# Kernel optimization log

Hardware: AMD Instinct MI355X
Metric: run time of the kernel (lower is better)

Reference implementation:

```python
import jax, jax.numpy as jnp
import numpy as np

EPS = 0.25  # diffusion-map epsilon

def setup_inputs() -> dict:
    key = jax.random.key(0)
    ks = jax.random.split(key, 6)
    B, N, F, L = 8, 2048, 256, 16
    s = lambda fan_in: 1.0 / np.sqrt(fan_in)
    return {
        "x":      jax.random.normal(ks[0], (B, N, F), dtype=jnp.float32),
        "proj_w": jax.random.normal(ks[1], (L, F), dtype=jnp.float32) * s(F),
        "proj_b": jnp.zeros((L,), dtype=jnp.float32),
        "pi_w1":  jax.random.normal(ks[2], (F, L), dtype=jnp.float32) * s(L),
        "pi_b1":  jnp.zeros((F,), dtype=jnp.float32),
        "pi_w2":  jax.random.normal(ks[3], (1, F), dtype=jnp.float32) * s(F),
        "pi_b2":  jnp.zeros((1,), dtype=jnp.float32),
        "dt":     jnp.array([0.1], dtype=jnp.float32),
    }

def reference(x, proj_w, proj_b, pi_w1, pi_b1, pi_w2, pi_b2, dt):
    # z = proj(x): [B, N, L]
    z = jnp.einsum("bnf,lf->bnl", x, proj_w) + proj_b
    # pairwise squared distances via expansion (avoids [B,N,N,L] intermediate)
    sq = jnp.sum(z * z, axis=-1)                              # [B, N]
    gram = jnp.einsum("bnl,bml->bnm", z, z)                   # [B, N, N]
    d2 = jnp.maximum(sq[:, :, None] + sq[:, None, :] - 2.0 * gram, 0.0)
    K = jnp.exp(-d2 / (4.0 * EPS))                            # K_epsilon [B,N,N]
    q = jnp.sum(K, axis=2)                                    # q_epsilon_tilde [B,N]
    # pi(z): MLP 16 -> 256 -> 1 with ReLU then Sigmoid
    h = jax.nn.relu(jnp.einsum("bnl,fl->bnf", z, pi_w1) + pi_b1)
    pi_v = jax.nn.sigmoid(jnp.einsum("bnf,of->bno", h, pi_w2) + pi_b2)[..., 0]  # [B,N]
    # K_tilde = K @ diag(pi/q): scale columns
    Kt = K * (pi_v / q)[:, None, :]                            # [B,N,N]
    row = jnp.sum(Kt, axis=2) + 1e-5                           # diag of D_tilde
    # L = (1/eps) * D_tilde^{-1} K_tilde - I ; inverse of diagonal = reciprocal
    # L @ x computed without materializing identity:
    Lx = (1.0 / EPS) * jnp.einsum("bnm,bmf->bnf", Kt / row[:, :, None], x) - x
    return x + dt[0] * Lx
```

## Files before the change

### kernel.cpp

```cpp
#include <hip/hip_runtime.h>
#include <hip/hip_bf16.h>

#define BATCH 8
#define NN    2048
#define FF    256
#define LL    16

typedef float f32x4 __attribute__((ext_vector_type(4)));
typedef short s16x8 __attribute__((ext_vector_type(8)));

static __device__ __forceinline__ unsigned short f2bf(float f) {
    return __builtin_bit_cast(unsigned short, __float2bfloat16(f));
}
static __device__ __forceinline__ float bf2f(unsigned short u) {
    unsigned int x = ((unsigned int)u) << 16;
    return __builtin_bit_cast(float, x);
}

typedef const __attribute__((address_space(1))) unsigned int glb_uint;
typedef __attribute__((address_space(3))) unsigned int lds_uint;
static __device__ __forceinline__ void gload_lds16(const void* g, void* l) {
    __builtin_amdgcn_global_load_lds((glb_uint*)g, (lds_uint*)l, 16, 0, 0);
}

__global__ __launch_bounds__(256) void fused_a_kernel(
    const float* __restrict__ x,
    const float* __restrict__ proj_w, const float* __restrict__ proj_b,
    const float* __restrict__ pi_w1,  const float* __restrict__ pi_b1,
    const float* __restrict__ pi_w2,  const float* __restrict__ pi_b2,
    unsigned short* __restrict__ xT,
    unsigned short* __restrict__ zbG,
    float* __restrict__ sqbuf,
    float* __restrict__ pibuf)
{
    const int bid = blockIdx.x;
    const int b = bid & 7, nt = bid >> 3;
    const int n0 = nt * 64;
    const int t = threadIdx.x;
    const int wv = t >> 6, ln = t & 63;

    const float* xb = x + (size_t)b * NN * FF;
    unsigned short* xTb = xT + (size_t)b * FF * NN;

    __shared__ unsigned short xbsh[64 * 264];
    __shared__ unsigned short Wbsh[16 * 264];
    __shared__ unsigned short W1bsh[256 * 24];
    __shared__ unsigned short zbsh[64 * 24];
    __shared__ float b1sh[256], w2sh[256], pbsh[16];

#pragma unroll
    for (int i = 0; i < 16; ++i) {
        const int idx = i * 256 + t;
        const int r = idx >> 6, cq = idx & 63;
        const float4 v = *(const float4*)(xb + (size_t)(n0 + r) * FF + cq * 4);
        ushort4 o; o.x = f2bf(v.x); o.y = f2bf(v.y); o.z = f2bf(v.z); o.w = f2bf(v.w);
        *(ushort4*)&xbsh[r * 264 + cq * 4] = o;
    }
    {
        const int l = t >> 4, fq = t & 15;
#pragma unroll
        for (int k2 = 0; k2 < 4; ++k2) {
            const float4 v = *(const float4*)(proj_w + l * FF + fq * 16 + k2 * 4);
            ushort4 o; o.x = f2bf(v.x); o.y = f2bf(v.y); o.z = f2bf(v.z); o.w = f2bf(v.w);
            *(ushort4*)&Wbsh[l * 264 + fq * 16 + k2 * 4] = o;
        }
    }
    {
#pragma unroll
        for (int k2 = 0; k2 < 4; ++k2) {
            const float4 v = *(const float4*)(pi_w1 + t * LL + k2 * 4);
            ushort4 o; o.x = f2bf(v.x); o.y = f2bf(v.y); o.z = f2bf(v.z); o.w = f2bf(v.w);
            *(ushort4*)&W1bsh[t * 24 + k2 * 4] = o;
        }
        b1sh[t] = pi_b1[t];
        w2sh[t] = pi_w2[t];
        if (t < 16) pbsh[t] = proj_b[t];
    }
    __syncthreads();

    f32x4 zacc = {0.f, 0.f, 0.f, 0.f};
#pragma unroll
    for (int g = 0; g < 8; ++g) {
        const s16x8 af = *(const s16x8*)&xbsh[(wv * 16 + (ln & 15)) * 264 + g * 32 + (ln >> 4) * 8];
        const s16x8 bf = *(const s16x8*)&Wbsh[(ln & 15) * 264 + g * 32 + (ln >> 4) * 8];
        zacc = __builtin_amdgcn_mfma_f32_16x16x32_bf16(af, bf, zacc, 0, 0, 0);
    }
    {
        const float pb = pbsh[ln & 15];
#pragma unroll
        for (int r = 0; r < 4; ++r) {
            const float zv = zacc[r] + pb;
            zbsh[(wv * 16 + (ln >> 4) * 4 + r) * 24 + (ln & 15)] = f2bf(zv);
        }
    }
    __syncthreads();

    if (t < 64) {
        unsigned short zr[16];
        float sq = 0.f;
#pragma unroll
        for (int l = 0; l < 16; ++l) {
            zr[l] = zbsh[t * 24 + l];
            const float zf = bf2f(zr[l]);
            sq = fmaf(zf, zf, sq);
        }
        const size_t gz = ((size_t)b * NN + n0 + t) * 16;
#pragma unroll
        for (int q4 = 0; q4 < 4; ++q4)
            *(ushort4*)(zbG + gz + q4 * 4) = *(ushort4*)&zr[q4 * 4];
        sqbuf[(size_t)b * NN + n0 + t] = sq;
    }

    {
        s16x8 bz = {0, 0, 0, 0, 0, 0, 0, 0};
        if ((ln >> 4) < 2)
            bz = *(const s16x8*)&zbsh[(wv * 16 + (ln & 15)) * 24 + (ln >> 4) * 8];
        float pisum = 0.f;
        const f32x4 zf4 = {0.f, 0.f, 0.f, 0.f};
#pragma unroll
        for (int ft = 0; ft < 16; ++ft) {
            s16x8 aw = {0, 0, 0, 0, 0, 0, 0, 0};
            if ((ln >> 4) < 2)
                aw = *(const s16x8*)&W1bsh[(ft * 16 + (ln & 15)) * 24 + (ln >> 4) * 8];
            const f32x4 h4 = __builtin_amdgcn_mfma_f32_16x16x32_bf16(aw, bz, zf4, 0, 0, 0);
#pragma unroll
            for (int r = 0; r < 4; ++r) {
                const int f = ft * 16 + (ln >> 4) * 4 + r;
                float h = h4[r] + b1sh[f];
                h = fmaxf(h, 0.f);
                pisum = fmaf(h, w2sh[f], pisum);
            }
        }
        pisum += __shfl_xor(pisum, 16, 64);
        pisum += __shfl_xor(pisum, 32, 64);
        if (ln < 16) {
            const float tp = pisum + pi_b2[0];
            pibuf[(size_t)b * NN + n0 + wv * 16 + ln] = 1.f / (1.f + __expf(-tp));
        }
    }

    {
        const int foff = wv * 64;
#pragma unroll
        for (int ff = 0; ff < 64; ++ff) {
            const unsigned short v = xbsh[ln * 264 + foff + ff];
            xTb[(size_t)(foff + ff) * NN + n0 + ln] = v;
        }
    }
}

__global__ __launch_bounds__(256) void qc_kernel(
    const unsigned short* __restrict__ zbG,
    const float* __restrict__ sqbuf,
    const float* __restrict__ pibuf,
    float* __restrict__ cbuf)
{
    const int bid = blockIdx.x;
    const int b = bid & 7, nt = bid >> 3;
    const int n0 = nt * 64;
    const int t = threadIdx.x;
    const int wv = t >> 6, ln = t & 63;

    const unsigned short* zb = zbG + (size_t)b * NN * LL;
    const float* sqb = sqbuf + (size_t)b * NN;

    __shared__ unsigned short zq[2][256 * 24];
    __shared__ float sqq[2][256];

    s16x8 af = {0, 0, 0, 0, 0, 0, 0, 0};
    if ((ln >> 4) < 2)
        af = *(const s16x8*)(zb + (size_t)(n0 + wv * 16 + (ln & 15)) * 16 + (ln >> 4) * 8);
    float sqn[4];
#pragma unroll
    for (int r = 0; r < 4; ++r) sqn[r] = sqb[n0 + wv * 16 + (ln >> 4) * 4 + r];

    float S[4] = {0.f, 0.f, 0.f, 0.f};
    const f32x4 zf4 = {0.f, 0.f, 0.f, 0.f};

    uint4 za, zc; float sv;
    za = *(const uint4*)(zb + (size_t)t * 16);
    zc = *(const uint4*)(zb + (size_t)t * 16 + 8);
    sv = sqb[t];
    *(uint4*)&zq[0][t * 24] = za;
    *(uint4*)&zq[0][t * 24 + 8] = zc;
    sqq[0][t] = sv;
    __syncthreads();

    for (int ch = 0; ch < 8; ++ch) {
        const int cur = ch & 1;
        if (ch < 7) {
            const int m = (ch + 1) * 256 + t;
            za = *(const uint4*)(zb + (size_t)m * 16);
            zc = *(const uint4*)(zb + (size_t)m * 16 + 8);
            sv = sqb[m];
        }
#pragma unroll
        for (int mt = 0; mt < 16; ++mt) {
            const int mloc = mt * 16 + (ln & 15);
            s16x8 bf = {0, 0, 0, 0, 0, 0, 0, 0};
            if ((ln >> 4) < 2)
                bf = *(const s16x8*)&zq[cur][mloc * 24 + (ln >> 4) * 8];
            const f32x4 g = __builtin_amdgcn_mfma_f32_16x16x32_bf16(af, bf, zf4, 0, 0, 0);
            const float sqm = sqq[cur][mloc];
#pragma unroll
            for (int r = 0; r < 4; ++r)
                S[r] += __expf(2.f * g[r] - sqn[r] - sqm);
        }
        if (ch < 7) {
            *(uint4*)&zq[cur ^ 1][t * 24] = za;
            *(uint4*)&zq[cur ^ 1][t * 24 + 8] = zc;
            sqq[cur ^ 1][t] = sv;
        }
        __syncthreads();
    }
#pragma unroll
    for (int r = 0; r < 4; ++r) {
        S[r] += __shfl_xor(S[r], 1, 64);
        S[r] += __shfl_xor(S[r], 2, 64);
        S[r] += __shfl_xor(S[r], 4, 64);
        S[r] += __shfl_xor(S[r], 8, 64);
    }
    if ((ln & 15) == 0) {
#pragma unroll
        for (int r = 0; r < 4; ++r) {
            const int n = n0 + wv * 16 + (ln >> 4) * 4 + r;
            const size_t gi = (size_t)b * NN + n;
            cbuf[gi] = pibuf[gi] / S[r];
        }
    }
}

__global__ __launch_bounds__(512) void main_kernel(
    const float* __restrict__ x,
    const unsigned short* __restrict__ xT,
    const unsigned short* __restrict__ zbG,
    const float* __restrict__ sqbuf,
    const float* __restrict__ cbuf,
    const float* __restrict__ dtp,
    float* __restrict__ out)
{
    const int bid = blockIdx.x;
    const int b = bid & 7, nt = bid >> 3;
    const int n0 = nt * 64;
    const int t = threadIdx.x;
    const int wv = t >> 6, ln = t & 63;

    const float*          xb  = x   + (size_t)b * NN * FF;
    const unsigned short* xTb = xT  + (size_t)b * FF * NN;
    const unsigned short* zb  = zbG + (size_t)b * NN * LL;
    const float*          sqB = sqbuf + (size_t)b * NN;
    const float*          cB  = cbuf  + (size_t)b * NN;
    float*                ob  = out + (size_t)b * NN * FF;

    __shared__ unsigned short xsh[2 * 16384];
    __shared__ unsigned short wsh[2 * 4096];
    __shared__ unsigned short zsh[2 * 64 * 24];
    __shared__ float csh[2][64], sqh[2][64];
    __shared__ float rsp[2][64];

    const float dtv = dtp[0];
    const int ntile = wv >> 1;

    s16x8 af = {0, 0, 0, 0, 0, 0, 0, 0};
    if ((ln >> 4) < 2)
        af = *(const s16x8*)(zb + (size_t)(n0 + ntile * 16 + (ln & 15)) * 16 + (ln >> 4) * 8);
    float sqn[4];
#pragma unroll
    for (int r = 0; r < 4; ++r) sqn[r] = sqB[n0 + ntile * 16 + (ln >> 4) * 4 + r];

    f32x4 acc[2][4];
#pragma unroll
    for (int fi = 0; fi < 2; ++fi)
#pragma unroll
        for (int ni = 0; ni < 4; ++ni) acc[fi][ni] = (f32x4){0.f, 0.f, 0.f, 0.f};
    float rloc[4] = {0.f, 0.f, 0.f, 0.f};
    const f32x4 zf4 = {0.f, 0.f, 0.f, 0.f};

    uint4 zreg; float creg = 0.f, sreg = 0.f;

    if (t < 128) {
        const int m = t >> 1, half = t & 1;
        zreg = *(const uint4*)(zb + (size_t)m * 16 + half * 8);
        *(uint4*)&zsh[m * 24 + half * 8] = zreg;
    } else if (t < 192) {
        csh[0][t - 128] = cB[t - 128];
    } else if (t < 256) {
        sqh[0][t - 192] = sqB[t - 192];
    }
#pragma unroll
    for (int i = 0; i < 4; ++i) {
        const int floc = i * 8 + (ln >> 3);
        const int cp = ln & 7;
        const int cl = cp ^ (floc & 7);
        const unsigned short* src = xTb + (size_t)(wv * 32 + floc) * NN + cl * 8;
        gload_lds16(src, (char*)xsh + wv * 4096 + i * 1024);
    }
    __syncthreads();

    for (int kt = 0; kt < 32; ++kt) {
        const int cur = kt & 1;
        unsigned short* zc = zsh + cur * (64 * 24);
        unsigned short* wc = wsh + cur * 4096;
        const unsigned short* xc = xsh + cur * 16384;

        if (kt < 31) {
            const int m1 = (kt + 1) * 64;
            if (t < 128) {
                const int m = t >> 1, half = t & 1;
                zreg = *(const uint4*)(zb + (size_t)(m1 + m) * 16 + half * 8);
            } else if (t < 192) creg = cB[m1 + t - 128];
            else if (t < 256)   sreg = sqB[m1 + t - 192];
        }

#pragma unroll
        for (int mi = 0; mi < 2; ++mi) {
            const int mt = (wv & 1) * 2 + mi;
            const int mloc = mt * 16 + (ln & 15);
            s16x8 bf = {0, 0, 0, 0, 0, 0, 0, 0};
            if ((ln >> 4) < 2)
                bf = *(const s16x8*)&zc[mloc * 24 + (ln >> 4) * 8];
            const f32x4 g = __builtin_amdgcn_mfma_f32_16x16x32_bf16(af, bf, zf4, 0, 0, 0);
            const float sqm = sqh[cur][mloc], cm = csh[cur][mloc];
#pragma unroll
            for (int r = 0; r < 4; ++r) {
                const float e = 2.f * g[r] - sqn[r] - sqm;
                const float wf = __expf(e) * cm;
                rloc[r] += wf;
                const int nr = ntile * 16 + (ln >> 4) * 4 + r;
                const int phys = (mloc >> 3) ^ (nr & 7);
                wc[nr * 64 + phys * 8 + (mloc & 7)] = f2bf(wf);
            }
        }

        if (kt < 31) {
            unsigned short* zn = zsh + (cur ^ 1) * (64 * 24);
            if (t < 128) {
                const int m = t >> 1, half = t & 1;
                *(uint4*)&zn[m * 24 + half * 8] = zreg;
            } else if (t < 192) csh[cur ^ 1][t - 128] = creg;
            else if (t < 256)   sqh[cur ^ 1][t - 192] = sreg;
        }
        __syncthreads();

        if (kt < 31) {
            const int m1 = (kt + 1) * 64;
            char* xn = (char*)xsh + (cur ^ 1) * 32768;
#pragma unroll
            for (int i = 0; i < 4; ++i) {
                const int floc = i * 8 + (ln >> 3);
                const int cp = ln & 7;
                const int cl = cp ^ (floc & 7);
                const unsigned short* src = xTb + (size_t)(wv * 32 + floc) * NN + m1 + cl * 8;
                gload_lds16(src, xn + wv * 4096 + i * 1024);
            }
        }
        __builtin_amdgcn_sched_barrier(0);

#pragma unroll
        for (int ks = 0; ks < 2; ++ks) {
            s16x8 a2[2], bw[4];
#pragma unroll
            for (int fi = 0; fi < 2; ++fi) {
                const int floc = fi * 16 + (ln & 15);
                const int phys = (ks * 4 + (ln >> 4)) ^ (floc & 7);
                a2[fi] = *(const s16x8*)&xc[wv * 2048 + floc * 64 + phys * 8];
            }
#pragma unroll
            for (int ni = 0; ni < 4; ++ni) {
                const int nr2 = ni * 16 + (ln & 15);
                const int phys = (ks * 4 + (ln >> 4)) ^ (nr2 & 7);
                bw[ni] = *(const s16x8*)&wc[nr2 * 64 + phys * 8];
            }
#pragma unroll
            for (int fi = 0; fi < 2; ++fi)
#pragma unroll
                for (int ni = 0; ni < 4; ++ni)
                    acc[fi][ni] = __builtin_amdgcn_mfma_f32_16x16x32_bf16(
                        a2[fi], bw[ni], acc[fi][ni], 0, 0, 0);
        }
    }

#pragma unroll
    for (int r = 0; r < 4; ++r) {
        rloc[r] += __shfl_xor(rloc[r], 1, 64);
        rloc[r] += __shfl_xor(rloc[r], 2, 64);
        rloc[r] += __shfl_xor(rloc[r], 4, 64);
        rloc[r] += __shfl_xor(rloc[r], 8, 64);
    }
    if ((ln & 15) == 0) {
#pragma unroll
        for (int r = 0; r < 4; ++r)
            rsp[wv & 1][ntile * 16 + (ln >> 4) * 4 + r] = rloc[r];
    }
    __syncthreads();

#pragma unroll
    for (int ni = 0; ni < 4; ++ni) {
        const int nr = ni * 16 + (ln & 15);
        const float rstot = rsp[0][nr] + rsp[1][nr] + 1e-5f;
        const float sc = 4.f * dtv / rstot;
        const int ng = n0 + nr;
#pragma unroll
        for (int fi = 0; fi < 2; ++fi) {
            const int fg = wv * 32 + fi * 16 + (ln >> 4) * 4;
            const float4 xv = *(const float4*)(xb + (size_t)ng * FF + fg);
            float4 o;
            o.x = (1.f - dtv) * xv.x + sc * acc[fi][ni][0];
            o.y = (1.f - dtv) * xv.y + sc * acc[fi][ni][1];
            o.z = (1.f - dtv) * xv.z + sc * acc[fi][ni][2];
            o.w = (1.f - dtv) * xv.w + sc * acc[fi][ni][3];
            *(float4*)(ob + (size_t)ng * FF + fg) = o;
        }
    }
}

extern "C" void kernel_launch(void* const* d_in, const int* in_sizes, int n_in,
                              void* d_out, int out_size, void* d_ws, size_t ws_size,
                              hipStream_t stream) {
    const float* x      = (const float*)d_in[0];
    const float* proj_w = (const float*)d_in[1];
    const float* proj_b = (const float*)d_in[2];
    const float* pi_w1  = (const float*)d_in[3];
    const float* pi_b1  = (const float*)d_in[4];
    const float* pi_w2  = (const float*)d_in[5];
    const float* pi_b2  = (const float*)d_in[6];
    const float* dtp    = (const float*)d_in[7];
    float* out = (float*)d_out;

    unsigned short* xT  = (unsigned short*)d_ws;
    unsigned short* zbG = xT + (size_t)BATCH * FF * NN;
    float* sqbuf = (float*)(zbG + (size_t)BATCH * NN * LL);
    float* pibuf = sqbuf + (size_t)BATCH * NN;
    float* cbuf  = pibuf + (size_t)BATCH * NN;

    fused_a_kernel<<<dim3(BATCH * (NN / 64)), dim3(256), 0, stream>>>(
        x, proj_w, proj_b, pi_w1, pi_b1, pi_w2, pi_b2, xT, zbG, sqbuf, pibuf);

    qc_kernel<<<dim3(BATCH * (NN / 64)), dim3(256), 0, stream>>>(
        zbG, sqbuf, pibuf, cbuf);

    main_kernel<<<dim3(BATCH * (NN / 64)), dim3(512), 0, stream>>>(
        x, xT, zbG, sqbuf, cbuf, dtp, out);
}
```

Measured before the change: 149.6 us.

## Restructure all three kernels: smaller tiles, direct global loads, register-prefetched main loop

New measurement: 153.8 us. +2.8%, slower.

```diff
diff --git a/kernel.cpp b/kernel.cpp
--- a/kernel.cpp
+++ b/kernel.cpp
@@ -15,12 +15,6 @@
 static __device__ __forceinline__ float bf2f(unsigned short u) {
     unsigned int x = ((unsigned int)u) << 16;
     return __builtin_bit_cast(float, x);
-}
-
-typedef const __attribute__((address_space(1))) unsigned int glb_uint;
-typedef __attribute__((address_space(3))) unsigned int lds_uint;
-static __device__ __forceinline__ void gload_lds16(const void* g, void* l) {
-    __builtin_amdgcn_global_load_lds((glb_uint*)g, (lds_uint*)l, 16, 0, 0);
 }
 
 __global__ __launch_bounds__(256) void fused_a_kernel(
@@ -35,117 +29,119 @@
 {
     const int bid = blockIdx.x;
     const int b = bid & 7, nt = bid >> 3;
-    const int n0 = nt * 64;
+    const int n0 = nt * 32;
     const int t = threadIdx.x;
     const int wv = t >> 6, ln = t & 63;
+    const int kg = ln >> 4, cl = ln & 15;
 
     const float* xb = x + (size_t)b * NN * FF;
     unsigned short* xTb = xT + (size_t)b * FF * NN;
 
-    __shared__ unsigned short xbsh[64 * 264];
+    __shared__ unsigned short xbsh[32 * 264];
     __shared__ unsigned short Wbsh[16 * 264];
     __shared__ unsigned short W1bsh[256 * 24];
-    __shared__ unsigned short zbsh[64 * 24];
+    __shared__ unsigned short zbsh[32 * 24];
     __shared__ float b1sh[256], w2sh[256], pbsh[16];
-
-#pragma unroll
-    for (int i = 0; i < 16; ++i) {
-        const int idx = i * 256 + t;
-        const int r = idx >> 6, cq = idx & 63;
-        const float4 v = *(const float4*)(xb + (size_t)(n0 + r) * FF + cq * 4);
+    __shared__ float pp[2][32];
+
+#pragma unroll
+    for (int i = 0; i < 8; ++i) {
+        const int slot = i * 256 + t;
+        const int r = slot >> 6, c4 = slot & 63;
+        const float4 v = *(const float4*)(xb + (size_t)(n0 + r) * FF + c4 * 4);
         ushort4 o; o.x = f2bf(v.x); o.y = f2bf(v.y); o.z = f2bf(v.z); o.w = f2bf(v.w);
-        *(ushort4*)&xbsh[r * 264 + cq * 4] = o;
-    }
-    {
-        const int l = t >> 4, fq = t & 15;
-#pragma unroll
-        for (int k2 = 0; k2 < 4; ++k2) {
-            const float4 v = *(const float4*)(proj_w + l * FF + fq * 16 + k2 * 4);
-            ushort4 o; o.x = f2bf(v.x); o.y = f2bf(v.y); o.z = f2bf(v.z); o.w = f2bf(v.w);
-            *(ushort4*)&Wbsh[l * 264 + fq * 16 + k2 * 4] = o;
-        }
-    }
-    {
-#pragma unroll
-        for (int k2 = 0; k2 < 4; ++k2) {
-            const float4 v = *(const float4*)(pi_w1 + t * LL + k2 * 4);
-            ushort4 o; o.x = f2bf(v.x); o.y = f2bf(v.y); o.z = f2bf(v.z); o.w = f2bf(v.w);
-            *(ushort4*)&W1bsh[t * 24 + k2 * 4] = o;
-        }
-        b1sh[t] = pi_b1[t];
-        w2sh[t] = pi_w2[t];
-        if (t < 16) pbsh[t] = proj_b[t];
-    }
-    __syncthreads();
-
-    f32x4 zacc = {0.f, 0.f, 0.f, 0.f};
-#pragma unroll
-    for (int g = 0; g < 8; ++g) {
-        const s16x8 af = *(const s16x8*)&xbsh[(wv * 16 + (ln & 15)) * 264 + g * 32 + (ln >> 4) * 8];
-        const s16x8 bf = *(const s16x8*)&Wbsh[(ln & 15) * 264 + g * 32 + (ln >> 4) * 8];
-        zacc = __builtin_amdgcn_mfma_f32_16x16x32_bf16(af, bf, zacc, 0, 0, 0);
-    }
-    {
-        const float pb = pbsh[ln & 15];
-#pragma unroll
-        for (int r = 0; r < 4; ++r) {
-            const float zv = zacc[r] + pb;
-            zbsh[(wv * 16 + (ln >> 4) * 4 + r) * 24 + (ln & 15)] = f2bf(zv);
-        }
-    }
-    __syncthreads();
-
-    if (t < 64) {
-        unsigned short zr[16];
-        float sq = 0.f;
+        *(ushort4*)&xbsh[r * 264 + c4 * 4] = o;
+    }
+#pragma unroll
+    for (int i = 0; i < 4; ++i) {
+        const int slot = i * 256 + t;
+        const int l = slot >> 6, c4 = slot & 63;
+        const float4 v = *(const float4*)(proj_w + l * FF + c4 * 4);
+        ushort4 o; o.x = f2bf(v.x); o.y = f2bf(v.y); o.z = f2bf(v.z); o.w = f2bf(v.w);
+        *(ushort4*)&Wbsh[l * 264 + c4 * 4] = o;
+    }
+#pragma unroll
+    for (int i = 0; i < 4; ++i) {
+        const int slot = i * 256 + t;
+        const int f = slot >> 2, q = slot & 3;
+        const float4 v = *(const float4*)(pi_w1 + f * LL + q * 4);
+        ushort4 o; o.x = f2bf(v.x); o.y = f2bf(v.y); o.z = f2bf(v.z); o.w = f2bf(v.w);
+        *(ushort4*)&W1bsh[f * 24 + q * 4] = o;
+    }
+    b1sh[t] = pi_b1[t];
+    w2sh[t] = pi_w2[t];
+    if (t < 16) pbsh[t] = proj_b[t];
+    __syncthreads();
+
+    if (wv < 2) {
+        f32x4 zacc = {0.f, 0.f, 0.f, 0.f};
+#pragma unroll
+        for (int g = 0; g < 8; ++g) {
+            const s16x8 af = *(const s16x8*)&xbsh[(wv * 16 + cl) * 264 + g * 32 + kg * 8];
+            const s16x8 bf = *(const s16x8*)&Wbsh[cl * 264 + g * 32 + kg * 8];
+            zacc = __builtin_amdgcn_mfma_f32_16x16x32_bf16(af, bf, zacc, 0, 0, 0);
+        }
+        const float pb = pbsh[cl];
+#pragma unroll
+        for (int r = 0; r < 4; ++r)
+            zbsh[(wv * 16 + kg * 4 + r) * 24 + cl] = f2bf(zacc[r] + pb);
+    }
+    __syncthreads();
+
+    if (t < 32) {
+        unsigned short zr[16]; float sq = 0.f;
 #pragma unroll
         for (int l = 0; l < 16; ++l) {
             zr[l] = zbsh[t * 24 + l];
             const float zf = bf2f(zr[l]);
             sq = fmaf(zf, zf, sq);
         }
-        const size_t gz = ((size_t)b * NN + n0 + t) * 16;
-#pragma unroll
-        for (int q4 = 0; q4 < 4; ++q4)
-            *(ushort4*)(zbG + gz + q4 * 4) = *(ushort4*)&zr[q4 * 4];
+        unsigned short* dst = zbG + ((size_t)b * NN + n0 + t) * 16;
+        *(uint4*)dst = *(uint4*)&zr[0];
+        *(uint4*)(dst + 8) = *(uint4*)&zr[8];
         sqbuf[(size_t)b * NN + n0 + t] = sq;
     }
 
     {
+        const int ntl = wv & 1;
         s16x8 bz = {0, 0, 0, 0, 0, 0, 0, 0};
-        if ((ln >> 4) < 2)
-            bz = *(const s16x8*)&zbsh[(wv * 16 + (ln & 15)) * 24 + (ln >> 4) * 8];
+        if (kg < 2) bz = *(const s16x8*)&zbsh[(ntl * 16 + cl) * 24 + kg * 8];
         float pisum = 0.f;
         const f32x4 zf4 = {0.f, 0.f, 0.f, 0.f};
 #pragma unroll
-        for (int ft = 0; ft < 16; ++ft) {
+        for (int j = 0; j < 8; ++j) {
+            const int ft = (wv >> 1) * 8 + j;
             s16x8 aw = {0, 0, 0, 0, 0, 0, 0, 0};
-            if ((ln >> 4) < 2)
-                aw = *(const s16x8*)&W1bsh[(ft * 16 + (ln & 15)) * 24 + (ln >> 4) * 8];
+            if (kg < 2) aw = *(const s16x8*)&W1bsh[(ft * 16 + cl) * 24 + kg * 8];
             const f32x4 h4 = __builtin_amdgcn_mfma_f32_16x16x32_bf16(aw, bz, zf4, 0, 0, 0);
 #pragma unroll
             for (int r = 0; r < 4; ++r) {
-                const int f = ft * 16 + (ln >> 4) * 4 + r;
-                float h = h4[r] + b1sh[f];
-                h = fmaxf(h, 0.f);
+                const int f = ft * 16 + kg * 4 + r;
+                const float h = fmaxf(h4[r] + b1sh[f], 0.f);
                 pisum = fmaf(h, w2sh[f], pisum);
             }
         }
         pisum += __shfl_xor(pisum, 16, 64);
         pisum += __shfl_xor(pisum, 32, 64);
-        if (ln < 16) {
-            const float tp = pisum + pi_b2[0];
-            pibuf[(size_t)b * NN + n0 + wv * 16 + ln] = 1.f / (1.f + __expf(-tp));
-        }
-    }
-
-    {
-        const int foff = wv * 64;
-#pragma unroll
-        for (int ff = 0; ff < 64; ++ff) {
-            const unsigned short v = xbsh[ln * 264 + foff + ff];
-            xTb[(size_t)(foff + ff) * NN + n0 + ln] = v;
-        }
+        if (ln < 16) pp[wv >> 1][ntl * 16 + ln] = pisum;
+    }
+    __syncthreads();
+
+    if (t < 32) {
+        const float tp = pp[0][t] + pp[1][t] + pi_b2[0];
+        pibuf[(size_t)b * NN + n0 + t] = 1.f / (1.f + __expf(-tp));
+    }
+
+#pragma unroll
+    for (int it = 0; it < 8; ++it) {
+        const int f = wv * 64 + it * 8 + (ln >> 3);
+        const int q = ln & 7;
+        ushort4 o;
+        o.x = xbsh[(q * 4 + 0) * 264 + f];
+        o.y = xbsh[(q * 4 + 1) * 264 + f];
+        o.z = xbsh[(q * 4 + 2) * 264 + f];
+        o.w = xbsh[(q * 4 + 3) * 264 + f];
+        *(ushort4*)(xTb + (size_t)f * NN + n0 + q * 4) = o;
     }
 }
 
@@ -157,78 +153,50 @@
 {
     const int bid = blockIdx.x;
     const int b = bid & 7, nt = bid >> 3;
-    const int n0 = nt * 64;
+    const int n0 = nt * 32;
     const int t = threadIdx.x;
     const int wv = t >> 6, ln = t & 63;
+    const int kg = ln >> 4, cl = ln & 15;
 
     const unsigned short* zb = zbG + (size_t)b * NN * LL;
     const float* sqb = sqbuf + (size_t)b * NN;
-
-    __shared__ unsigned short zq[2][256 * 24];
-    __shared__ float sqq[2][256];
-
-    s16x8 af = {0, 0, 0, 0, 0, 0, 0, 0};
-    if ((ln >> 4) < 2)
-        af = *(const s16x8*)(zb + (size_t)(n0 + wv * 16 + (ln & 15)) * 16 + (ln >> 4) * 8);
-    float sqn[4];
-#pragma unroll
-    for (int r = 0; r < 4; ++r) sqn[r] = sqb[n0 + wv * 16 + (ln >> 4) * 4 + r];
-
-    float S[4] = {0.f, 0.f, 0.f, 0.f};
+    __shared__ float qq[2][32];
+
+    s16x8 zn = {0, 0, 0, 0, 0, 0, 0, 0};
+    if (kg < 2) zn = *(const s16x8*)(zb + (size_t)(n0 + (wv & 1) * 16 + cl) * 16 + kg * 8);
+    const float sqn = sqb[n0 + (wv & 1) * 16 + cl];
     const f32x4 zf4 = {0.f, 0.f, 0.f, 0.f};
-
-    uint4 za, zc; float sv;
-    za = *(const uint4*)(zb + (size_t)t * 16);
-    zc = *(const uint4*)(zb + (size_t)t * 16 + 8);
-    sv = sqb[t];
-    *(uint4*)&zq[0][t * 24] = za;
-    *(uint4*)&zq[0][t * 24 + 8] = zc;
-    sqq[0][t] = sv;
-    __syncthreads();
-
-    for (int ch = 0; ch < 8; ++ch) {
-        const int cur = ch & 1;
-        if (ch < 7) {
-            const int m = (ch + 1) * 256 + t;
-            za = *(const uint4*)(zb + (size_t)m * 16);
-            zc = *(const uint4*)(zb + (size_t)m * 16 + 8);
-            sv = sqb[m];
-        }
-#pragma unroll
-        for (int mt = 0; mt < 16; ++mt) {
-            const int mloc = mt * 16 + (ln & 15);
-            s16x8 bf = {0, 0, 0, 0, 0, 0, 0, 0};
-            if ((ln >> 4) < 2)
-                bf = *(const s16x8*)&zq[cur][mloc * 24 + (ln >> 4) * 8];
-            const f32x4 g = __builtin_amdgcn_mfma_f32_16x16x32_bf16(af, bf, zf4, 0, 0, 0);
-            const float sqm = sqq[cur][mloc];
+    float qloc = 0.f;
+
+#pragma unroll 2
+    for (int ch = 0; ch < 32; ++ch) {
+#pragma unroll
+        for (int mi = 0; mi < 2; ++mi) {
+            const int mm = ch * 64 + ((wv >> 1) + mi * 2) * 16;
+            s16x8 zm = {0, 0, 0, 0, 0, 0, 0, 0};
+            if (kg < 2) zm = *(const s16x8*)(zb + (size_t)(mm + cl) * 16 + kg * 8);
+            const f32x4 sqm4 = *(const f32x4*)(sqb + mm + kg * 4);
+            const f32x4 g = __builtin_amdgcn_mfma_f32_16x16x32_bf16(zm, zn, zf4, 0, 0, 0);
 #pragma unroll
             for (int r = 0; r < 4; ++r)
-                S[r] += __expf(2.f * g[r] - sqn[r] - sqm);
-        }
-        if (ch < 7) {
-            *(uint4*)&zq[cur ^ 1][t * 24] = za;
-            *(uint4*)&zq[cur ^ 1][t * 24 + 8] = zc;
-            sqq[cur ^ 1][t] = sv;
-        }
-        __syncthreads();
-    }
-#pragma unroll
-    for (int r = 0; r < 4; ++r) {
-        S[r] += __shfl_xor(S[r], 1, 64);
-        S[r] += __shfl_xor(S[r], 2, 64);
-        S[r] += __shfl_xor(S[r], 4, 64);
-        S[r] += __shfl_xor(S[r], 8, 64);
-    }
-    if ((ln & 15) == 0) {
-#pragma unroll
-        for (int r = 0; r < 4; ++r) {
-            const int n = n0 + wv * 16 + (ln >> 4) * 4 + r;
-            const size_t gi = (size_t)b * NN + n;
-            cbuf[gi] = pibuf[gi] / S[r];
-        }
-    }
-}
+                qloc += __expf(2.f * g[r] - sqm4[r] - sqn);
+        }
+    }
+    qloc += __shfl_xor(qloc, 16, 64);
+    qloc += __shfl_xor(qloc, 32, 64);
+    if (ln < 16) qq[wv >> 1][(wv & 1) * 16 + ln] = qloc;
+    __syncthreads();
+    if (t < 32) {
+        const size_t gi = (size_t)b * NN + n0 + t;
+        cbuf[gi] = pibuf[gi] / (qq[0][t] + qq[1][t]);
+    }
+}
+
+struct MRegs {
+    s16x8 zm0, zm1;
+    f32x4 sqm0, sqm1, cm0, cm1;
+    s16x8 a0, a1, a2, a3;
+};
 
 __global__ __launch_bounds__(512) void main_kernel(
     const float* __restrict__ x,
@@ -244,6 +212,9 @@
     const int n0 = nt * 64;
     const int t = threadIdx.x;
     const int wv = t >> 6, ln = t & 63;
+    const int kg = ln >> 4, cl = ln & 15;
+    const int nt4 = wv >> 1;
+    const int mgrp = wv & 1;
 
     const float*          xb  = x   + (size_t)b * NN * FF;
     const unsigned short* xTb = xT  + (size_t)b * FF * NN;
@@ -252,157 +223,117 @@
     const float*          cB  = cbuf  + (size_t)b * NN;
     float*                ob  = out + (size_t)b * NN * FF;
 
-    __shared__ unsigned short xsh[2 * 16384];
-    __shared__ unsigned short wsh[2 * 4096];
-    __shared__ unsigned short zsh[2 * 64 * 24];
-    __shared__ float csh[2][64], sqh[2][64];
+    __shared__ unsigned short wsh[2][64][64];
     __shared__ float rsp[2][64];
 
     const float dtv = dtp[0];
-    const int ntile = wv >> 1;
-
-    s16x8 af = {0, 0, 0, 0, 0, 0, 0, 0};
-    if ((ln >> 4) < 2)
-        af = *(const s16x8*)(zb + (size_t)(n0 + ntile * 16 + (ln & 15)) * 16 + (ln >> 4) * 8);
-    float sqn[4];
-#pragma unroll
-    for (int r = 0; r < 4; ++r) sqn[r] = sqB[n0 + ntile * 16 + (ln >> 4) * 4 + r];
+    const int nloc = nt4 * 16 + cl;
+
+    s16x8 zn = {0, 0, 0, 0, 0, 0, 0, 0};
+    if (kg < 2) zn = *(const s16x8*)(zb + (size_t)(n0 + nloc) * 16 + kg * 8);
+    const float sqn = sqB[n0 + nloc];
+    const f32x4 zf4 = {0.f, 0.f, 0.f, 0.f};
 
     f32x4 acc[2][4];
 #pragma unroll
     for (int fi = 0; fi < 2; ++fi)
 #pragma unroll
         for (int ni = 0; ni < 4; ++ni) acc[fi][ni] = (f32x4){0.f, 0.f, 0.f, 0.f};
-    float rloc[4] = {0.f, 0.f, 0.f, 0.f};
-    const f32x4 zf4 = {0.f, 0.f, 0.f, 0.f};
-
-    uint4 zreg; float creg = 0.f, sreg = 0.f;
-
-    if (t < 128) {
-        const int m = t >> 1, half = t & 1;
-        zreg = *(const uint4*)(zb + (size_t)m * 16 + half * 8);
-        *(uint4*)&zsh[m * 24 + half * 8] = zreg;
-    } else if (t < 192) {
-        csh[0][t - 128] = cB[t - 128];
-    } else if (t < 256) {
-        sqh[0][t - 192] = sqB[t - 192];
-    }
-#pragma unroll
-    for (int i = 0; i < 4; ++i) {
-        const int floc = i * 8 + (ln >> 3);
-        const int cp = ln & 7;
-        const int cl = cp ^ (floc & 7);
-        const unsigned short* src = xTb + (size_t)(wv * 32 + floc) * NN + cl * 8;
-        gload_lds16(src, (char*)xsh + wv * 4096 + i * 1024);
-    }
-    __syncthreads();
-
-    for (int kt = 0; kt < 32; ++kt) {
-        const int cur = kt & 1;
-        unsigned short* zc = zsh + cur * (64 * 24);
-        unsigned short* wc = wsh + cur * 4096;
-        const unsigned short* xc = xsh + cur * 16384;
-
-        if (kt < 31) {
-            const int m1 = (kt + 1) * 64;
-            if (t < 128) {
-                const int m = t >> 1, half = t & 1;
-                zreg = *(const uint4*)(zb + (size_t)(m1 + m) * 16 + half * 8);
-            } else if (t < 192) creg = cB[m1 + t - 128];
-            else if (t < 256)   sreg = sqB[m1 + t - 192];
-        }
-
-#pragma unroll
-        for (int mi = 0; mi < 2; ++mi) {
-            const int mt = (wv & 1) * 2 + mi;
-            const int mloc = mt * 16 + (ln & 15);
-            s16x8 bf = {0, 0, 0, 0, 0, 0, 0, 0};
-            if ((ln >> 4) < 2)
-                bf = *(const s16x8*)&zc[mloc * 24 + (ln >> 4) * 8];
-            const f32x4 g = __builtin_amdgcn_mfma_f32_16x16x32_bf16(af, bf, zf4, 0, 0, 0);
-            const float sqm = sqh[cur][mloc], cm = csh[cur][mloc];
-#pragma unroll
-            for (int r = 0; r < 4; ++r) {
-                const float e = 2.f * g[r] - sqn[r] - sqm;
-                const float wf = __expf(e) * cm;
-                rloc[r] += wf;
-                const int nr = ntile * 16 + (ln >> 4) * 4 + r;
-                const int phys = (mloc >> 3) ^ (nr & 7);
-                wc[nr * 64 + phys * 8 + (mloc & 7)] = f2bf(wf);
+    float rloc = 0.f;
+
+    auto PRE = [&](MRegs& R, int kt) {
+        const int m0 = kt * 64;
+        const int mmA = m0 + (mgrp * 2 + 0) * 16;
+        const int mmB = m0 + (mgrp * 2 + 1) * 16;
+        R.zm0 = (s16x8){0, 0, 0, 0, 0, 0, 0, 0};
+        R.zm1 = (s16x8){0, 0, 0, 0, 0, 0, 0, 0};
+        if (kg < 2) {
+            R.zm0 = *(const s16x8*)(zb + (size_t)(mmA + cl) * 16 + kg * 8);
+            R.zm1 = *(const s16x8*)(zb + (size_t)(mmB + cl) * 16 + kg * 8);
+        }
+        R.sqm0 = *(const f32x4*)(sqB + mmA + kg * 4);
+        R.sqm1 = *(const f32x4*)(sqB + mmB + kg * 4);
+        R.cm0  = *(const f32x4*)(cB + mmA + kg * 4);
+        R.cm1  = *(const f32x4*)(cB + mmB + kg * 4);
+        const unsigned short* xr0 = xTb + (size_t)(wv * 32 + cl) * NN + m0;
+        const unsigned short* xr1 = xTb + (size_t)(wv * 32 + 16 + cl) * NN + m0;
+        R.a0 = *(const s16x8*)(xr0 + kg * 8);
+        R.a1 = *(const s16x8*)(xr1 + kg * 8);
+        R.a2 = *(const s16x8*)(xr0 + 32 + kg * 8);
+        R.a3 = *(const s16x8*)(xr1 + 32 + kg * 8);
+    };
+
+    auto P1 = [&](const MRegs& R, int cur) {
+        char* wb = (char*)wsh + cur * 8192;
+#pragma unroll
+        for (int j = 0; j < 2; ++j) {
+            const s16x8 zm  = j ? R.zm1  : R.zm0;
+            const f32x4 sqm = j ? R.sqm1 : R.sqm0;
+            const f32x4 cm  = j ? R.cm1  : R.cm0;
+            const int mt = mgrp * 2 + j;
+            const f32x4 g = __builtin_amdgcn_mfma_f32_16x16x32_bf16(zm, zn, zf4, 0, 0, 0);
+            const float w0 = __expf(2.f * g[0] - sqm[0] - sqn) * cm[0];
+            const float w1 = __expf(2.f * g[1] - sqm[1] - sqn) * cm[1];
+            const float w2 = __expf(2.f * g[2] - sqm[2] - sqn) * cm[2];
+            const float w3 = __expf(2.f * g[3] - sqm[3] - sqn) * cm[3];
+            rloc += (w0 + w1) + (w2 + w3);
+            uint2 val;
+            val.x = (unsigned)f2bf(w0) | ((unsigned)f2bf(w1) << 16);
+            val.y = (unsigned)f2bf(w2) | ((unsigned)f2bf(w3) << 16);
+            const int c16 = mt * 2 + (kg >> 1);
+            const int phys = c16 ^ (nloc & 7);
+            *(uint2*)(wb + nloc * 128 + phys * 16 + (kg & 1) * 8) = val;
+        }
+    };
+
+    auto P2 = [&](const MRegs& R, int cur) {
+        const char* wb = (const char*)wsh + cur * 8192;
+#pragma unroll
+        for (int ks = 0; ks < 2; ++ks) {
+            s16x8 bw[4];
+#pragma unroll
+            for (int ni = 0; ni < 4; ++ni) {
+                const int nr = ni * 16 + cl;
+                const int phys = (ks * 4 + kg) ^ (nr & 7);
+                bw[ni] = *(const s16x8*)(wb + nr * 128 + phys * 16);
             }
-        }
-
-        if (kt < 31) {
-            unsigned short* zn = zsh + (cur ^ 1) * (64 * 24);
-            if (t < 128) {
-                const int m = t >> 1, half = t & 1;
-                *(uint4*)&zn[m * 24 + half * 8] = zreg;
-            } else if (t < 192) csh[cur ^ 1][t - 128] = creg;
-            else if (t < 256)   sqh[cur ^ 1][t - 192] = sreg;
-        }
+            const s16x8 aA = ks ? R.a2 : R.a0;
+            const s16x8 aB = ks ? R.a3 : R.a1;
+#pragma unroll
+            for (int ni = 0; ni < 4; ++ni) {
+                acc[0][ni] = __builtin_amdgcn_mfma_f32_16x16x32_bf16(aA, bw[ni], acc[0][ni], 0, 0, 0);
+                acc[1][ni] = __builtin_amdgcn_mfma_f32_16x16x32_bf16(aB, bw[ni], acc[1][ni], 0, 0, 0);
+            }
+        }
+    };
+
+    MRegs rA, rB;
+    PRE(rA, 0);
+    for (int kt2 = 0; kt2 < 32; kt2 += 2) {
+        PRE(rB, kt2 + 1);
+        P1(rA, 0);
         __syncthreads();
-
-        if (kt < 31) {
-            const int m1 = (kt + 1) * 64;
-            char* xn = (char*)xsh + (cur ^ 1) * 32768;
-#pragma unroll
-            for (int i = 0; i < 4; ++i) {
-                const int floc = i * 8 + (ln >> 3);
-                const int cp = ln & 7;
-                const int cl = cp ^ (floc & 7);
-                const unsigned short* src = xTb + (size_t)(wv * 32 + floc) * NN + m1 + cl * 8;
-                gload_lds16(src, xn + wv * 4096 + i * 1024);
-            }
-        }
-        __builtin_amdgcn_sched_barrier(0);
-
-#pragma unroll
-        for (int ks = 0; ks < 2; ++ks) {
-            s16x8 a2[2], bw[4];
-#pragma unroll
-            for (int fi = 0; fi < 2; ++fi) {
-                const int floc = fi * 16 + (ln & 15);
-                const int phys = (ks * 4 + (ln >> 4)) ^ (floc & 7);
-                a2[fi] = *(const s16x8*)&xc[wv * 2048 + floc * 64 + phys * 8];
-            }
-#pragma unroll
-            for (int ni = 0; ni < 4; ++ni) {
-                const int nr2 = ni * 16 + (ln & 15);
-                const int phys = (ks * 4 + (ln >> 4)) ^ (nr2 & 7);
-                bw[ni] = *(const s16x8*)&wc[nr2 * 64 + phys * 8];
-            }
-#pragma unroll
-            for (int fi = 0; fi < 2; ++fi)
-#pragma unroll
-                for (int ni = 0; ni < 4; ++ni)
-                    acc[fi][ni] = __builtin_amdgcn_mfma_f32_16x16x32_bf16(
-                        a2[fi], bw[ni], acc[fi][ni], 0, 0, 0);
-        }
-    }
-
-#pragma unroll
-    for (int r = 0; r < 4; ++r) {
-        rloc[r] += __shfl_xor(rloc[r], 1, 64);
-        rloc[r] += __shfl_xor(rloc[r], 2, 64);
-        rloc[r] += __shfl_xor(rloc[r], 4, 64);
-        rloc[r] += __shfl_xor(rloc[r], 8, 64);
-    }
-    if ((ln & 15) == 0) {
-#pragma unroll
-        for (int r = 0; r < 4; ++r)
-            rsp[wv & 1][ntile * 16 + (ln >> 4) * 4 + r] = rloc[r];
-    }
+        P2(rA, 0);
+        if (kt2 + 2 < 32) PRE(rA, kt2 + 2);
+        P1(rB, 1);
+        __syncthreads();
+        P2(rB, 1);
+    }
+
+    rloc += __shfl_xor(rloc, 16, 64);
+    rloc += __shfl_xor(rloc, 32, 64);
+    if (ln < 16) rsp[mgrp][nt4 * 16 + ln] = rloc;
     __syncthreads();
 
 #pragma unroll
     for (int ni = 0; ni < 4; ++ni) {
-        const int nr = ni * 16 + (ln & 15);
-        const float rstot = rsp[0][nr] + rsp[1][nr] + 1e-5f;
+        const int nl = ni * 16 + cl;
+        const float rstot = rsp[0][nl] + rsp[1][nl] + 1e-5f;
         const float sc = 4.f * dtv / rstot;
-        const int ng = n0 + nr;
+        const int ng = n0 + nl;
 #pragma unroll
         for (int fi = 0; fi < 2; ++fi) {
-            const int fg = wv * 32 + fi * 16 + (ln >> 4) * 4;
+            const int fg = wv * 32 + fi * 16 + kg * 4;
             const float4 xv = *(const float4*)(xb + (size_t)ng * FF + fg);
             float4 o;
             o.x = (1.f - dtv) * xv.x + sc * acc[fi][ni][0];
@@ -433,10 +364,10 @@
     float* pibuf = sqbuf + (size_t)BATCH * NN;
     float* cbuf  = pibuf + (size_t)BATCH * NN;
 
-    fused_a_kernel<<<dim3(BATCH * (NN / 64)), dim3(256), 0, stream>>>(
+    fused_a_kernel<<<dim3(BATCH * (NN / 32)), dim3(256), 0, stream>>>(
         x, proj_w, proj_b, pi_w1, pi_b1, pi_w2, pi_b2, xT, zbG, sqbuf, pibuf);
 
-    qc_kernel<<<dim3(BATCH * (NN / 64)), dim3(256), 0, stream>>>(
+    qc_kernel<<<dim3(BATCH * (NN / 32)), dim3(256), 0, stream>>>(
         zbG, sqbuf, pibuf, cbuf);
 
     main_kernel<<<dim3(BATCH * (NN / 64)), dim3(512), 0, stream>>>(
```
